# Performance work log

Hardware: AMD Instinct MI355X
Metric: run time of the kernel (lower is better)

Reference implementation:

```python
import jax, jax.numpy as jnp
import numpy as np

EMBED_DIM = 1024
NUM_TOKENS = 32
TOKEN_DIM = 32  # ceil(1024/32)
CODEBOOK_SIZE = 256
BATCH = 32768
BETA = 0.25


def setup_inputs() -> dict:
    key = jax.random.key(0)
    ks = jax.random.split(key, 6)
    lim_e = 1.0 / np.sqrt(EMBED_DIM)
    lim_d = 1.0 / np.sqrt(NUM_TOKENS * TOKEN_DIM)
    lim_c = 1.0 / CODEBOOK_SIZE
    return {
        "skills": jax.random.normal(ks[0], (BATCH, EMBED_DIM), jnp.float32),
        "enc_w": jax.random.uniform(ks[1], (NUM_TOKENS * TOKEN_DIM, EMBED_DIM), jnp.float32, -lim_e, lim_e),
        "enc_b": jax.random.uniform(ks[2], (NUM_TOKENS * TOKEN_DIM,), jnp.float32, -lim_e, lim_e),
        "codebook": jax.random.uniform(ks[3], (CODEBOOK_SIZE, TOKEN_DIM), jnp.float32, -lim_c, lim_c),
        "dec_w": jax.random.uniform(ks[4], (EMBED_DIM, NUM_TOKENS * TOKEN_DIM), jnp.float32, -lim_d, lim_d),
        "dec_b": jax.random.uniform(ks[5], (EMBED_DIM,), jnp.float32, -lim_d, lim_d),
    }


def reference(skills, enc_w, enc_b, codebook, dec_w, dec_b):
    B = skills.shape[0]
    # encoder linear -> [B, num_tokens, token_dim]
    projected = (skills @ enc_w.T + enc_b).reshape(B, NUM_TOKENS, TOKEN_DIM)
    flat = projected.reshape(-1, TOKEN_DIM)  # [B*T, d]
    # squared-euclidean distances to codebook entries: [B*T, K]
    dists = (
        jnp.sum(flat * flat, axis=1, keepdims=True)
        - 2.0 * flat @ codebook.T
        + jnp.sum(codebook * codebook, axis=1)[None, :]
    )
    codes = jnp.argmin(dists, axis=1)  # [B*T]
    quantized = codebook[codes].reshape(B, NUM_TOKENS, TOKEN_DIM)
    # straight-through estimator
    st = projected + jax.lax.stop_gradient(quantized - projected)
    commitment = jnp.mean((projected - jax.lax.stop_gradient(quantized)) ** 2)
    codebook_loss = jnp.mean((quantized - jax.lax.stop_gradient(projected)) ** 2)
    vq_loss = codebook_loss + BETA * commitment
    reconstructed = st.reshape(B, NUM_TOKENS * TOKEN_DIM) @ dec_w.T + dec_b
    recon_loss = jnp.mean((reconstructed - skills) ** 2)
    loss = vq_loss + recon_loss
    return reconstructed, codes.reshape(B, NUM_TOKENS), loss
```

## Files before the change

kernel.cpp:

```cpp
#include <hip/hip_runtime.h>
#include <hip/hip_bf16.h>
#include <float.h>

#define OUT_CODES_OFF (33554432UL)
#define OUT_LOSS_OFF  (34603008UL)
#define TAU 1e-5f
#define INV_N (1.0f/33554432.0f)

typedef __attribute__((ext_vector_type(8))) short s16x8;
typedef __attribute__((ext_vector_type(4))) float f32x4;

__device__ __forceinline__ unsigned short bf16r(float x) {
    unsigned int u = __float_as_uint(x);
    unsigned int r = (u + 0x7FFFu + ((u >> 16) & 1u)) >> 16;
    return (unsigned short)r;
}
__device__ __forceinline__ float bf16f(unsigned short h) {
    return __uint_as_float(((unsigned int)h) << 16);
}
__device__ __forceinline__ void split8r(float4 v0, float4 v1, s16x8& h, s16x8& l) {
    float xs[8] = {v0.x, v0.y, v0.z, v0.w, v1.x, v1.y, v1.z, v1.w};
    #pragma unroll
    for (int e = 0; e < 8; ++e) {
        unsigned int u = __float_as_uint(xs[e]);
        unsigned short hh = (unsigned short)(u >> 16);
        h[e] = (short)hh;
        l[e] = (short)bf16r(xs[e] - bf16f(hh));
    }
}

__global__ void k_prep_r(const float* __restrict__ in,
                         unsigned short* __restrict__ o,
                         int n8)
{
    const int i = blockIdx.x * 256 + threadIdx.x;
    if (i >= n8) return;
    const float4* p = (const float4*)(in + (size_t)i * 8);
    float4 v0 = p[0], v1 = p[1];
    float xs[8] = {v0.x, v0.y, v0.z, v0.w, v1.x, v1.y, v1.z, v1.w};
    s16x8 h;
    #pragma unroll
    for (int e = 0; e < 8; ++e) h[e] = (short)bf16r(xs[e]);
    *(s16x8*)(o + (size_t)i * 8) = h;
}

__launch_bounds__(512, 1)
__global__ void k_enc(const float* __restrict__ skills,
                      const float* __restrict__ enc_w,
                      const float* __restrict__ enc_b,
                      const float* __restrict__ cb_g,
                      float* __restrict__ out)
{
    __shared__ __align__(16) unsigned short us[40960];

    const int tid = threadIdx.x;
    const int rb = blockIdx.x >> 1, chf = blockIdx.x & 1;
    const int r0 = rb * 128;
    const int wid = tid >> 6, lane = tid & 63;
    const int wm = wid >> 1, wn = wid & 1;
    const int mbase = wm * 32;
    const int lhi = lane >> 4, llo = lane & 15;
    const int srow = tid >> 2, sq = tid & 3;

    if (tid < 256) {
        const float4* cr = (const float4*)&cb_g[tid * 32];
        float s = 0.f;
        #pragma unroll
        for (int i = 0; i < 8; ++i) {
            float4 v = cr[i];
            float c[4] = {v.x, v.y, v.z, v.w};
            #pragma unroll
            for (int e = 0; e < 4; ++e) {
                const int d = i * 4 + e;
                unsigned int u = __float_as_uint(c[e]);
                unsigned short hh = (unsigned short)(u >> 16);
                us[20480 + tid * 40 + d] = hh;
                us[30720 + tid * 40 + d] = bf16r(c[e] - bf16f(hh));
                s = fmaf(c[e], c[e], s);
            }
        }
        *(float*)&us[20480 + tid * 40 + 32] = s;
    }
    __syncthreads();

    float vq_local = 0.f;
    f32x4 acc[2][4];
    float4 ra0, ra1, rb0, rb1;

    {
        const float* ap = &skills[(size_t)(r0 + srow) * 1024 + sq * 8];
        ra0 = *(const float4*)ap; ra1 = *(const float4*)(ap + 4);
        const float* bp = &enc_w[(size_t)(chf * 512 + srow) * 1024 + sq * 8];
        rb0 = *(const float4*)bp; rb1 = *(const float4*)(bp + 4);
    }

    for (int it = 0; it < 128; ++it) {
        const int nt = it >> 5, kt = it & 31;
        if (kt == 0) {
            #pragma unroll
            for (int mf = 0; mf < 2; ++mf)
                #pragma unroll
                for (int nf = 0; nf < 4; ++nf) acc[mf][nf] = (f32x4)0.f;
        }
        __syncthreads();
        {
            s16x8 h, l;
            split8r(ra0, ra1, h, l);
            *(s16x8*)&us[srow * 40 + sq * 8] = h;
            *(s16x8*)&us[5120 + srow * 40 + sq * 8] = l;
            split8r(rb0, rb1, h, l);
            *(s16x8*)&us[10240 + srow * 40 + sq * 8] = h;
            *(s16x8*)&us[15360 + srow * 40 + sq * 8] = l;
        }
        __syncthreads();
        if (it < 127) {
            const int it2 = it + 1, nt2 = it2 >> 5, kt2 = it2 & 31;
            const float* ap = &skills[(size_t)(r0 + srow) * 1024 + kt2 * 32 + sq * 8];
            ra0 = *(const float4*)ap; ra1 = *(const float4*)(ap + 4);
            const float* bp = &enc_w[(size_t)(chf * 512 + nt2 * 128 + srow) * 1024 + kt2 * 32 + sq * 8];
            rb0 = *(const float4*)bp; rb1 = *(const float4*)(bp + 4);
        }
        {
            s16x8 ah[2], al[2];
            #pragma unroll
            for (int mf = 0; mf < 2; ++mf) {
                const int row = mbase + mf * 16 + llo;
                ah[mf] = *(s16x8*)&us[row * 40 + lhi * 8];
                al[mf] = *(s16x8*)&us[5120 + row * 40 + lhi * 8];
            }
            #pragma unroll
            for (int nf = 0; nf < 4; ++nf) {
                const int rowb = wn * 64 + nf * 16 + llo;
                s16x8 bh = *(s16x8*)&us[10240 + rowb * 40 + lhi * 8];
                s16x8 bl = *(s16x8*)&us[15360 + rowb * 40 + lhi * 8];
                #pragma unroll
                for (int mf = 0; mf < 2; ++mf) {
                    acc[mf][nf] = __builtin_amdgcn_mfma_f32_16x16x32_bf16(ah[mf], bh, acc[mf][nf], 0, 0, 0);
                    acc[mf][nf] = __builtin_amdgcn_mfma_f32_16x16x32_bf16(ah[mf], bl, acc[mf][nf], 0, 0, 0);
                    acc[mf][nf] = __builtin_amdgcn_mfma_f32_16x16x32_bf16(al[mf], bh, acc[mf][nf], 0, 0, 0);
                }
            }
        }

        if (kt == 31) {
            for (int c = 0; c < 2; ++c) {
                __syncthreads();
                if (wn == c) {
                    #pragma unroll
                    for (int nf = 0; nf < 4; ++nf) {
                        const int colh = nf * 16 + llo;
                        const int tlc = colh >> 5, d = colh & 31;
                        const float bias = enc_b[chf * 512 + nt * 128 + c * 64 + colh];
                        #pragma unroll
                        for (int mf = 0; mf < 2; ++mf)
                            #pragma unroll
                            for (int r = 0; r < 4; ++r) {
                                const int m_local = mbase + mf * 16 + lhi * 4 + r;
                                float val = acc[mf][nf][r] + bias;
                                unsigned int u = __float_as_uint(val);
                                unsigned short hh = (unsigned short)(u >> 16);
                                const int tok = m_local * 2 + tlc;
                                us[tok * 40 + d] = hh;
                                us[10240 + tok * 40 + d] = bf16r(val - bf16f(hh));
                            }
                    }
                }
                __syncthreads();
                #pragma unroll
                for (int gi = 0; gi < 2; ++gi) {
                    const int g = wid * 2 + gi;
                    const int tokrow = g * 16 + llo;
                    s16x8 fh = *(s16x8*)&us[tokrow * 40 + lhi * 8];
                    s16x8 fl = *(s16x8*)&us[10240 + tokrow * 40 + lhi * 8];
                    float Fp = 0.f;
                    #pragma unroll
                    for (int e = 0; e < 8; ++e) {
                        float fv = bf16f((unsigned short)fh[e]) + bf16f((unsigned short)fl[e]);
                        Fp = fmaf(fv, fv, Fp);
                    }
                    Fp += __shfl_xor(Fp, 16);
                    Fp += __shfl_xor(Fp, 32);

                    float s1[4], s2[4]; int bj[4];
                    #pragma unroll
                    for (int r = 0; r < 4; ++r) { s1[r] = FLT_MAX; s2[r] = FLT_MAX; bj[r] = 0; }
                    for (int jb = 0; jb < 16; ++jb) {
                        const int j = jb * 16 + llo;
                        s16x8 ch = *(s16x8*)&us[20480 + j * 40 + lhi * 8];
                        s16x8 cl = *(s16x8*)&us[30720 + j * 40 + lhi * 8];
                        const float cnv = *(const float*)&us[20480 + j * 40 + 32];
                        f32x4 sc = (f32x4)0.f;
                        sc = __builtin_amdgcn_mfma_f32_16x16x32_bf16(fh, ch, sc, 0, 0, 0);
                        sc = __builtin_amdgcn_mfma_f32_16x16x32_bf16(fh, cl, sc, 0, 0, 0);
                        sc = __builtin_amdgcn_mfma_f32_16x16x32_bf16(fl, ch, sc, 0, 0, 0);
                        #pragma unroll
                        for (int r = 0; r < 4; ++r) {
                            float s = fmaf(-2.f, sc[r], cnv);
                            if (s < s1[r])      { s2[r] = s1[r]; s1[r] = s; bj[r] = j; }
                            else if (s < s2[r]) { s2[r] = s; }
                        }
                    }
                    #pragma unroll
                    for (int r = 0; r < 4; ++r) {
                        float a1 = s1[r], a2 = s2[r]; int aj = bj[r];
                        #pragma unroll
                        for (int off = 1; off <= 8; off <<= 1) {
                            float o1 = __shfl_xor(a1, off);
                            float o2 = __shfl_xor(a2, off);
                            int   oj = __shfl_xor(aj, off);
                            if (o1 < a1) { a2 = fminf(a1, o2); a1 = o1; aj = oj; }
                            else         { a2 = fminf(o1, a2); }
                        }
                        const float Ft = __shfl(Fp, lhi * 4 + r);
                        if (llo == 0) {
                            const int tok_local = g * 16 + lhi * 4 + r;
                            const int row = tok_local >> 1, tlc2 = tok_local & 1;
                            const int t = chf * 16 + nt * 4 + c * 2 + tlc2;
                            float cv = (a2 - a1 < TAU) ? (float)(aj + 512) : (float)aj;
                            out[OUT_CODES_OFF + (size_t)(r0 + row) * 32 + t] = cv;
                            vq_local += Ft + a1;
                        }
                    }
                }
            }
        }
    }
    {
        float v = vq_local;
        #pragma unroll
        for (int off = 32; off >= 1; off >>= 1) v += __shfl_xor(v, off);
        if (lane == 0) atomicAdd(&out[OUT_LOSS_OFF], v * (1.25f * INV_N));
    }
}

__launch_bounds__(256)
__global__ void k_fix(const float* __restrict__ skills,
                      const float* __restrict__ enc_w,
                      const float* __restrict__ enc_b,
                      const float* __restrict__ cb_g,
                      float* __restrict__ codes)
{
    __shared__ unsigned int cnt;
    __shared__ unsigned short list[256];

    const int tid = threadIdx.x;
    const int base = blockIdx.x * 256;

    if (tid == 0) cnt = 0;
    __syncthreads();
    {
        const int c = (int)codes[base + tid];
        if (c >= 512) {
            unsigned int ix = atomicAdd(&cnt, 1u);
            list[ix] = (unsigned short)tid;
        }
    }
    __syncthreads();
    const unsigned int n = cnt;
    if (n == 0) return;

    const int wv = tid >> 6, lane = tid & 63;
    const int d = lane & 31;

    for (unsigned int i = wv; i < n; i += 4) {
        const int tok = base + (int)list[i];
        const int row = tok >> 5;
        const int t   = tok & 31;

        const float4* s4 = (const float4*)&skills[(size_t)row * 1024];
        const float4* w4 = (const float4*)&enc_w[(size_t)(t * 32 + d) * 1024];
        float v1 = 0.f, v2 = 0.f, v3 = 0.f;
        for (int q = 0; q < 96; ++q) {
            float4 a = s4[q], b = w4[q];
            v1 = fmaf(a.x, b.x, v1); v1 = fmaf(a.y, b.y, v1);
            v1 = fmaf(a.z, b.z, v1); v1 = fmaf(a.w, b.w, v1);
        }
        for (int q = 96; q < 192; ++q) {
            float4 a = s4[q], b = w4[q];
            v2 = fmaf(a.x, b.x, v2); v2 = fmaf(a.y, b.y, v2);
            v2 = fmaf(a.z, b.z, v2); v2 = fmaf(a.w, b.w, v2);
        }
        for (int q = 192; q < 256; ++q) {
            float4 a = s4[q], b = w4[q];
            v3 = fmaf(a.x, b.x, v3); v3 = fmaf(a.y, b.y, v3);
            v3 = fmaf(a.z, b.z, v3); v3 = fmaf(a.w, b.w, v3);
        }
        const float pd = ((v1 + v2) + v3) + enc_b[t * 32 + d];

        float pv[32];
        #pragma unroll
        for (int dd = 0; dd < 32; ++dd) pv[dd] = __shfl(pd, dd);

        float F;
        {
            float s[32];
            #pragma unroll
            for (int dd = 0; dd < 32; ++dd) s[dd] = pv[dd] * pv[dd];
            float r[8];
            #pragma unroll
            for (int j = 0; j < 8; ++j) r[j] = ((s[j] + s[8+j]) + s[16+j]) + s[24+j];
            F = ((r[0] + r[1]) + (r[2] + r[3])) + ((r[4] + r[5]) + (r[6] + r[7]));
        }

        float bs = FLT_MAX; int bj = 0;
        for (int m = 0; m < 4; ++m) {
            const int j = m * 64 + lane;
            const float* cj = &cb_g[j * 32];
            float g = 0.f;
            #pragma unroll
            for (int dd = 0; dd < 32; ++dd) g = fmaf(pv[dd], cj[dd], g);
            float cs[32];
            #pragma unroll
            for (int dd = 0; dd < 32; ++dd) cs[dd] = cj[dd] * cj[dd];
            float r[8];
            #pragma unroll
            for (int jj = 0; jj < 8; ++jj) r[jj] = ((cs[jj] + cs[8+jj]) + cs[16+jj]) + cs[24+jj];
            float cn = ((r[0] + r[1]) + (r[2] + r[3])) + ((r[4] + r[5]) + (r[6] + r[7]));
            float dist = (F - 2.0f * g) + cn;
            if (dist < bs) { bs = dist; bj = j; }
        }
        #pragma unroll
        for (int off = 32; off >= 1; off >>= 1) {
            float os = __shfl_xor(bs, off);
            int   oj = __shfl_xor(bj, off);
            if (os < bs || (os == bs && oj < bj)) { bs = os; bj = oj; }
        }
        if (lane == 0) codes[tok] = (float)bj;
    }
}

template <bool PRED>
__launch_bounds__(512)
__global__ void k_dec(const float* __restrict__ skills,
                      const float* __restrict__ cb_g,
                      const unsigned short* __restrict__ cbb,
                      const float* __restrict__ dec_w,
                      const unsigned short* __restrict__ dwb,
                      const float* __restrict__ dec_b,
                      const float* __restrict__ codes,
                      float* __restrict__ recon,
                      float* __restrict__ loss_out)
{
    __shared__ unsigned short Qt[128][40], Wt[128][40];

    const int tid = threadIdx.x;
    const int r0 = (blockIdx.x >> 3) * 128;
    const int n0 = (blockIdx.x & 7) * 128;
    const int wid = tid >> 6, lane = tid & 63;
    const int wm = wid >> 1, wn = wid & 1;
    const int mbase = wm * 32, nbase = wn * 64;
    const int lhi = lane >> 4, llo = lane & 15;
    const int srow = tid >> 2, sq = tid & 3;

    f32x4 acc[2][4];
    #pragma unroll
    for (int mf = 0; mf < 2; ++mf)
        #pragma unroll
        for (int nf = 0; nf < 4; ++nf) acc[mf][nf] = (f32x4)0.f;

    s16x8 q16, w16;
    float4 q0, q1, w0, w1;
    int cnext;
    {
        const int c0 = ((int)codes[(size_t)(r0 + srow) * 32 + 0]) & 255;
        if (PRED) {
            q16 = *(const s16x8*)(cbb + c0 * 32 + sq * 8);
            w16 = *(const s16x8*)(dwb + (size_t)(n0 + srow) * 1024 + sq * 8);
        } else {
            const float* cp = &cb_g[c0 * 32 + sq * 8];
            q0 = *(const float4*)cp; q1 = *(const float4*)(cp + 4);
            const float* wp = &dec_w[(size_t)(n0 + srow) * 1024 + sq * 8];
            w0 = *(const float4*)wp; w1 = *(const float4*)(wp + 4);
        }
        cnext = ((int)codes[(size_t)(r0 + srow) * 32 + 1]) & 255;
    }

    for (int t = 0; t < 32; ++t) {
        __syncthreads();
        if (PRED) {
            *(s16x8*)&Qt[srow][sq * 8] = q16;
            *(s16x8*)&Wt[srow][sq * 8] = w16;
        } else {
            float xs[8] = {q0.x, q0.y, q0.z, q0.w, q1.x, q1.y, q1.z, q1.w};
            s16x8 h;
            #pragma unroll
            for (int e = 0; e < 8; ++e) h[e] = (short)bf16r(xs[e]);
            *(s16x8*)&Qt[srow][sq * 8] = h;
            float ys[8] = {w0.x, w0.y, w0.z, w0.w, w1.x, w1.y, w1.z, w1.w};
            #pragma unroll
            for (int e = 0; e < 8; ++e) h[e] = (short)bf16r(ys[e]);
            *(s16x8*)&Wt[srow][sq * 8] = h;
        }
        __syncthreads();
        if (t < 31) {
            if (PRED) {
                q16 = *(const s16x8*)(cbb + cnext * 32 + sq * 8);
                w16 = *(const s16x8*)(dwb + (size_t)(n0 + srow) * 1024 + (t + 1) * 32 + sq * 8);
            } else {
                const float* cp = &cb_g[cnext * 32 + sq * 8];
                q0 = *(const float4*)cp; q1 = *(const float4*)(cp + 4);
                const float* wp = &dec_w[(size_t)(n0 + srow) * 1024 + (t + 1) * 32 + sq * 8];
                w0 = *(const float4*)wp; w1 = *(const float4*)(wp + 4);
            }
            if (t < 30) cnext = ((int)codes[(size_t)(r0 + srow) * 32 + t + 2]) & 255;
        }
        s16x8 aq[2], bw[4];
        #pragma unroll
        for (int mf = 0; mf < 2; ++mf)
            aq[mf] = *(s16x8*)&Qt[mbase + mf * 16 + llo][lhi * 8];
        #pragma unroll
        for (int nf = 0; nf < 4; ++nf)
            bw[nf] = *(s16x8*)&Wt[nbase + nf * 16 + llo][lhi * 8];
        #pragma unroll
        for (int mf = 0; mf < 2; ++mf)
            #pragma unroll
            for (int nf = 0; nf < 4; ++nf)
                acc[mf][nf] = __builtin_amdgcn_mfma_f32_16x16x32_bf16(aq[mf], bw[nf], acc[mf][nf], 0, 0, 0);
    }

    float lsum = 0.f;
    #pragma unroll
    for (int mf = 0; mf < 2; ++mf)
        #pragma unroll
        for (int nf = 0; nf < 4; ++nf) {
            const int col = n0 + nbase + nf * 16 + llo;
            const float bias = dec_b[col];
            #pragma unroll
            for (int r = 0; r < 4; ++r) {
                const int row = r0 + mbase + mf * 16 + lhi * 4 + r;
                float rv = acc[mf][nf][r] + bias;
                float dv = rv - skills[(size_t)row * 1024 + col];
                lsum = fmaf(dv, dv, lsum);
                recon[(size_t)row * 1024 + col] = rv;
            }
        }
    #pragma unroll
    for (int off = 32; off >= 1; off >>= 1) lsum += __shfl_xor(lsum, off);
    if (lane == 0) atomicAdd(loss_out, lsum * INV_N);
}

extern "C" void kernel_launch(void* const* d_in, const int* in_sizes, int n_in,
                              void* d_out, int out_size, void* d_ws, size_t ws_size,
                              hipStream_t stream)
{
    const float* skills = (const float*)d_in[0];
    const float* enc_w  = (const float*)d_in[1];
    const float* enc_b  = (const float*)d_in[2];
    const float* cbg    = (const float*)d_in[3];
    const float* dec_w  = (const float*)d_in[4];
    const float* dec_b  = (const float*)d_in[5];
    float* out = (float*)d_out;

    hipMemsetAsync(out + OUT_LOSS_OFF, 0, 4, stream);
    k_enc<<<dim3(512), dim3(512), 0, stream>>>(skills, enc_w, enc_b, cbg, out);
    k_fix<<<dim3(4096), dim3(256), 0, stream>>>(skills, enc_w, enc_b, cbg, out + OUT_CODES_OFF);

    const bool pred = (ws_size >= (2097152UL + 16384UL + 64UL));
    unsigned short* dwb = (unsigned short*)d_ws;
    unsigned short* cbb = dwb + 1048576UL;
    if (pred) {
        k_prep_r<<<dim3(512), dim3(256), 0, stream>>>(dec_w, dwb, 131072);
        k_prep_r<<<dim3(4), dim3(256), 0, stream>>>(cbg, cbb, 1024);
        k_dec<true><<<dim3(2048), dim3(512), 0, stream>>>(skills, cbg, cbb, dec_w, dwb, dec_b,
                                                          out + OUT_CODES_OFF, out, out + OUT_LOSS_OFF);
    } else {
        k_dec<false><<<dim3(2048), dim3(512), 0, stream>>>(skills, cbg, cbb, dec_w, dwb, dec_b,
                                                           out + OUT_CODES_OFF, out, out + OUT_LOSS_OFF);
    }
}
```

Before: 922.4 us.

## Halve encoder N-tile to 64 columns and interleave two token groups in codebook search

The encoder GEMM N-tile per block shrinks from 128 to 64 columns, so the outer loop runs 256 iterations instead of 128 and only half the threads load enc_w. The epilogue now handles one 64-column slice per tile with a single staging pass, and the codebook search processes both token groups per warp inside one loop over codebook entries, sharing the codebook LDS loads. This cuts accumulator registers and simplifies the epilogue. In exchange, the skills tile is reloaded and re-split twice as often, so activation traffic and conversion work double.

Result: slower. 1.064 ms (+15.3%).

```diff
diff --git a/kernel.cpp b/kernel.cpp
--- a/kernel.cpp
+++ b/kernel.cpp
@@ -61,6 +61,7 @@
     const int mbase = wm * 32;
     const int lhi = lane >> 4, llo = lane & 15;
     const int srow = tid >> 2, sq = tid & 3;
+    const int brow = (tid & 255) >> 2;
 
     if (tid < 256) {
         const float4* cr = (const float4*)&cb_g[tid * 32];
@@ -84,23 +85,25 @@
     __syncthreads();
 
     float vq_local = 0.f;
-    f32x4 acc[2][4];
+    f32x4 acc[2][2];
     float4 ra0, ra1, rb0, rb1;
 
     {
         const float* ap = &skills[(size_t)(r0 + srow) * 1024 + sq * 8];
         ra0 = *(const float4*)ap; ra1 = *(const float4*)(ap + 4);
-        const float* bp = &enc_w[(size_t)(chf * 512 + srow) * 1024 + sq * 8];
-        rb0 = *(const float4*)bp; rb1 = *(const float4*)(bp + 4);
-    }
-
-    for (int it = 0; it < 128; ++it) {
+        if (tid < 256) {
+            const float* bp = &enc_w[(size_t)(chf * 512 + brow) * 1024 + sq * 8];
+            rb0 = *(const float4*)bp; rb1 = *(const float4*)(bp + 4);
+        }
+    }
+
+    for (int it = 0; it < 256; ++it) {
         const int nt = it >> 5, kt = it & 31;
         if (kt == 0) {
             #pragma unroll
             for (int mf = 0; mf < 2; ++mf)
                 #pragma unroll
-                for (int nf = 0; nf < 4; ++nf) acc[mf][nf] = (f32x4)0.f;
+                for (int nf = 0; nf < 2; ++nf) acc[mf][nf] = (f32x4)0.f;
         }
         __syncthreads();
         {
@@ -108,17 +111,21 @@
             split8r(ra0, ra1, h, l);
             *(s16x8*)&us[srow * 40 + sq * 8] = h;
             *(s16x8*)&us[5120 + srow * 40 + sq * 8] = l;
-            split8r(rb0, rb1, h, l);
-            *(s16x8*)&us[10240 + srow * 40 + sq * 8] = h;
-            *(s16x8*)&us[15360 + srow * 40 + sq * 8] = l;
+            if (tid < 256) {
+                split8r(rb0, rb1, h, l);
+                *(s16x8*)&us[10240 + brow * 40 + sq * 8] = h;
+                *(s16x8*)&us[12800 + brow * 40 + sq * 8] = l;
+            }
         }
         __syncthreads();
-        if (it < 127) {
+        if (it < 255) {
             const int it2 = it + 1, nt2 = it2 >> 5, kt2 = it2 & 31;
             const float* ap = &skills[(size_t)(r0 + srow) * 1024 + kt2 * 32 + sq * 8];
             ra0 = *(const float4*)ap; ra1 = *(const float4*)(ap + 4);
-            const float* bp = &enc_w[(size_t)(chf * 512 + nt2 * 128 + srow) * 1024 + kt2 * 32 + sq * 8];
-            rb0 = *(const float4*)bp; rb1 = *(const float4*)(bp + 4);
+            if (tid < 256) {
+                const float* bp = &enc_w[(size_t)(chf * 512 + nt2 * 64 + brow) * 1024 + kt2 * 32 + sq * 8];
+                rb0 = *(const float4*)bp; rb1 = *(const float4*)(bp + 4);
+            }
         }
         {
             s16x8 ah[2], al[2];
@@ -129,10 +136,10 @@
                 al[mf] = *(s16x8*)&us[5120 + row * 40 + lhi * 8];
             }
             #pragma unroll
-            for (int nf = 0; nf < 4; ++nf) {
-                const int rowb = wn * 64 + nf * 16 + llo;
+            for (int nf = 0; nf < 2; ++nf) {
+                const int rowb = wn * 32 + nf * 16 + llo;
                 s16x8 bh = *(s16x8*)&us[10240 + rowb * 40 + lhi * 8];
-                s16x8 bl = *(s16x8*)&us[15360 + rowb * 40 + lhi * 8];
+                s16x8 bl = *(s16x8*)&us[12800 + rowb * 40 + lhi * 8];
                 #pragma unroll
                 for (int mf = 0; mf < 2; ++mf) {
                     acc[mf][nf] = __builtin_amdgcn_mfma_f32_16x16x32_bf16(ah[mf], bh, acc[mf][nf], 0, 0, 0);
@@ -143,83 +150,85 @@
         }
 
         if (kt == 31) {
-            for (int c = 0; c < 2; ++c) {
-                __syncthreads();
-                if (wn == c) {
+            __syncthreads();
+            #pragma unroll
+            for (int nf = 0; nf < 2; ++nf) {
+                const int d = nf * 16 + llo;
+                const float bias = enc_b[chf * 512 + nt * 64 + wn * 32 + d];
+                #pragma unroll
+                for (int mf = 0; mf < 2; ++mf)
                     #pragma unroll
-                    for (int nf = 0; nf < 4; ++nf) {
-                        const int colh = nf * 16 + llo;
-                        const int tlc = colh >> 5, d = colh & 31;
-                        const float bias = enc_b[chf * 512 + nt * 128 + c * 64 + colh];
-                        #pragma unroll
-                        for (int mf = 0; mf < 2; ++mf)
-                            #pragma unroll
-                            for (int r = 0; r < 4; ++r) {
-                                const int m_local = mbase + mf * 16 + lhi * 4 + r;
-                                float val = acc[mf][nf][r] + bias;
-                                unsigned int u = __float_as_uint(val);
-                                unsigned short hh = (unsigned short)(u >> 16);
-                                const int tok = m_local * 2 + tlc;
-                                us[tok * 40 + d] = hh;
-                                us[10240 + tok * 40 + d] = bf16r(val - bf16f(hh));
-                            }
+                    for (int r = 0; r < 4; ++r) {
+                        const int m_local = mbase + mf * 16 + lhi * 4 + r;
+                        float val = acc[mf][nf][r] + bias;
+                        unsigned int u = __float_as_uint(val);
+                        unsigned short hh = (unsigned short)(u >> 16);
+                        const int tok = m_local * 2 + wn;
+                        us[tok * 40 + d] = hh;
+                        us[10240 + tok * 40 + d] = bf16r(val - bf16f(hh));
+                    }
+            }
+            __syncthreads();
+            s16x8 fh[2], fl[2];
+            #pragma unroll
+            for (int gi = 0; gi < 2; ++gi) {
+                const int tokrow = (wid * 2 + gi) * 16 + llo;
+                fh[gi] = *(s16x8*)&us[tokrow * 40 + lhi * 8];
+                fl[gi] = *(s16x8*)&us[10240 + tokrow * 40 + lhi * 8];
+            }
+            float s1[2][4], s2[2][4]; int bj[2][4];
+            #pragma unroll
+            for (int gi = 0; gi < 2; ++gi)
+                #pragma unroll
+                for (int r = 0; r < 4; ++r) { s1[gi][r] = FLT_MAX; s2[gi][r] = FLT_MAX; bj[gi][r] = 0; }
+            for (int jb = 0; jb < 16; ++jb) {
+                const int j = jb * 16 + llo;
+                s16x8 ch = *(s16x8*)&us[20480 + j * 40 + lhi * 8];
+                s16x8 cl = *(s16x8*)&us[30720 + j * 40 + lhi * 8];
+                const float cnv = *(const float*)&us[20480 + j * 40 + 32];
+                #pragma unroll
+                for (int gi = 0; gi < 2; ++gi) {
+                    f32x4 sc = (f32x4)0.f;
+                    sc = __builtin_amdgcn_mfma_f32_16x16x32_bf16(fh[gi], ch, sc, 0, 0, 0);
+                    sc = __builtin_amdgcn_mfma_f32_16x16x32_bf16(fh[gi], cl, sc, 0, 0, 0);
+                    sc = __builtin_amdgcn_mfma_f32_16x16x32_bf16(fl[gi], ch, sc, 0, 0, 0);
+                    #pragma unroll
+                    for (int r = 0; r < 4; ++r) {
+                        float s = fmaf(-2.f, sc[r], cnv);
+                        if (s < s1[gi][r])      { s2[gi][r] = s1[gi][r]; s1[gi][r] = s; bj[gi][r] = j; }
+                        else if (s < s2[gi][r]) { s2[gi][r] = s; }
                     }
                 }
-                __syncthreads();
-                #pragma unroll
-                for (int gi = 0; gi < 2; ++gi) {
-                    const int g = wid * 2 + gi;
-                    const int tokrow = g * 16 + llo;
-                    s16x8 fh = *(s16x8*)&us[tokrow * 40 + lhi * 8];
-                    s16x8 fl = *(s16x8*)&us[10240 + tokrow * 40 + lhi * 8];
-                    float Fp = 0.f;
+            }
+            #pragma unroll
+            for (int gi = 0; gi < 2; ++gi) {
+                float Fp = 0.f;
+                #pragma unroll
+                for (int e = 0; e < 8; ++e) {
+                    float fv = bf16f((unsigned short)fh[gi][e]) + bf16f((unsigned short)fl[gi][e]);
+                    Fp = fmaf(fv, fv, Fp);
+                }
+                Fp += __shfl_xor(Fp, 16);
+                Fp += __shfl_xor(Fp, 32);
+                #pragma unroll
+                for (int r = 0; r < 4; ++r) {
+                    float a1 = s1[gi][r], a2 = s2[gi][r]; int aj = bj[gi][r];
                     #pragma unroll
-                    for (int e = 0; e < 8; ++e) {
-                        float fv = bf16f((unsigned short)fh[e]) + bf16f((unsigned short)fl[e]);
-                        Fp = fmaf(fv, fv, Fp);
+                    for (int off = 1; off <= 8; off <<= 1) {
+                        float o1 = __shfl_xor(a1, off);
+                        float o2 = __shfl_xor(a2, off);
+                        int   oj = __shfl_xor(aj, off);
+                        if (o1 < a1) { a2 = fminf(a1, o2); a1 = o1; aj = oj; }
+                        else         { a2 = fminf(o1, a2); }
                     }
-                    Fp += __shfl_xor(Fp, 16);
-                    Fp += __shfl_xor(Fp, 32);
-
-                    float s1[4], s2[4]; int bj[4];
-                    #pragma unroll
-                    for (int r = 0; r < 4; ++r) { s1[r] = FLT_MAX; s2[r] = FLT_MAX; bj[r] = 0; }
-                    for (int jb = 0; jb < 16; ++jb) {
-                        const int j = jb * 16 + llo;
-                        s16x8 ch = *(s16x8*)&us[20480 + j * 40 + lhi * 8];
-                        s16x8 cl = *(s16x8*)&us[30720 + j * 40 + lhi * 8];
-                        const float cnv = *(const float*)&us[20480 + j * 40 + 32];
-                        f32x4 sc = (f32x4)0.f;
-                        sc = __builtin_amdgcn_mfma_f32_16x16x32_bf16(fh, ch, sc, 0, 0, 0);
-                        sc = __builtin_amdgcn_mfma_f32_16x16x32_bf16(fh, cl, sc, 0, 0, 0);
-                        sc = __builtin_amdgcn_mfma_f32_16x16x32_bf16(fl, ch, sc, 0, 0, 0);
-                        #pragma unroll
-                        for (int r = 0; r < 4; ++r) {
-                            float s = fmaf(-2.f, sc[r], cnv);
-                            if (s < s1[r])      { s2[r] = s1[r]; s1[r] = s; bj[r] = j; }
-                            else if (s < s2[r]) { s2[r] = s; }
-                        }
-                    }
-                    #pragma unroll
-                    for (int r = 0; r < 4; ++r) {
-                        float a1 = s1[r], a2 = s2[r]; int aj = bj[r];
-                        #pragma unroll
-                        for (int off = 1; off <= 8; off <<= 1) {
-                            float o1 = __shfl_xor(a1, off);
-                            float o2 = __shfl_xor(a2, off);
-                            int   oj = __shfl_xor(aj, off);
-                            if (o1 < a1) { a2 = fminf(a1, o2); a1 = o1; aj = oj; }
-                            else         { a2 = fminf(o1, a2); }
-                        }
-                        const float Ft = __shfl(Fp, lhi * 4 + r);
-                        if (llo == 0) {
-                            const int tok_local = g * 16 + lhi * 4 + r;
-                            const int row = tok_local >> 1, tlc2 = tok_local & 1;
-                            const int t = chf * 16 + nt * 4 + c * 2 + tlc2;
-                            float cv = (a2 - a1 < TAU) ? (float)(aj + 512) : (float)aj;
-                            out[OUT_CODES_OFF + (size_t)(r0 + row) * 32 + t] = cv;
-                            vq_local += Ft + a1;
-                        }
+                    const float Ft = __shfl(Fp, lhi * 4 + r);
+                    if (llo == 0) {
+                        const int tok_local = (wid * 2 + gi) * 16 + lhi * 4 + r;
+                        const int row = tok_local >> 1;
+                        const int t = chf * 16 + nt * 2 + (tok_local & 1);
+                        float cv = (a2 - a1 < TAU) ? (float)(aj + 512) : (float)aj;
+                        out[OUT_CODES_OFF + (size_t)(r0 + row) * 32 + t] = cv;
+                        vq_local += Ft + a1;
                     }
                 }
             }
```

## Pre-split encoder operands to bf16 hi/lo tiles and load via global_load_lds

Applied to the files above, without the earlier changes.

Adds a prep kernel that splits skills and enc_w into bf16 hi/lo pairs laid out per tile. The encoder can then stream tiles straight into LDS with global_load_lds instead of loading fp32 and converting in-kernel. The split skills are stashed in the output buffer, and enc_w goes into a larger workspace. The codebook argmin loop is also restructured so two token groups share each codebook fragment load. In exchange the kernel gains an extra full pass over the 128MB skills input plus a 128MB bf16 write, and the path only runs when the workspace is large enough.

Result: no change. 914.4 us (-0.9%).

```diff
diff --git a/kernel.cpp b/kernel.cpp
--- a/kernel.cpp
+++ b/kernel.cpp
@@ -27,6 +27,26 @@
         h[e] = (short)hh;
         l[e] = (short)bf16r(xs[e] - bf16f(hh));
     }
+}
+
+__device__ __forceinline__ void gld16(const unsigned short* g, unsigned short* l) {
+    __builtin_amdgcn_global_load_lds(
+        (const __attribute__((address_space(1))) unsigned int*)g,
+        (__attribute__((address_space(3))) unsigned int*)l, 16, 0, 0);
+}
+
+__global__ void k_prep_split(const float* __restrict__ in,
+                             unsigned short* __restrict__ ot)
+{
+    const int b = blockIdx.x, tid = threadIdx.x;
+    const int rblk = b >> 5, kt = b & 31, r = tid >> 2, q = tid & 3;
+    const float* src = in + (size_t)(rblk * 128 + r) * 1024 + kt * 32 + q * 8;
+    float4 v0 = *(const float4*)src, v1 = *(const float4*)(src + 4);
+    s16x8 h, l;
+    split8r(v0, v1, h, l);
+    unsigned short* dst = ot + (size_t)b * 8192 + q * 1024 + r * 8;
+    *(s16x8*)dst = h;
+    *(s16x8*)(dst + 4096) = l;
 }
 
 __global__ void k_prep_r(const float* __restrict__ in,
@@ -45,11 +65,192 @@
 }
 
 __launch_bounds__(512, 1)
-__global__ void k_enc(const float* __restrict__ skills,
-                      const float* __restrict__ enc_w,
-                      const float* __restrict__ enc_b,
-                      const float* __restrict__ cb_g,
-                      float* __restrict__ out)
+__global__ void k_enc_gl(const unsigned short* __restrict__ At,
+                         const unsigned short* __restrict__ Bt,
+                         const float* __restrict__ enc_b,
+                         const float* __restrict__ cb_g,
+                         float* __restrict__ out)
+{
+    __shared__ __align__(16) unsigned short us[33280];
+
+    const int tid = threadIdx.x;
+    const int rb = blockIdx.x >> 1, chf = blockIdx.x & 1;
+    const int r0 = rb * 128;
+    const int wid = tid >> 6, lane = tid & 63;
+    const int wm = wid >> 1, wn = wid & 1;
+    const int mbase = wm * 32;
+    const int lhi = lane >> 4, llo = lane & 15;
+
+    if (tid < 256) {
+        const float4* cr = (const float4*)&cb_g[tid * 32];
+        float s = 0.f;
+        #pragma unroll
+        for (int i = 0; i < 8; ++i) {
+            float4 v = cr[i];
+            float c[4] = {v.x, v.y, v.z, v.w};
+            #pragma unroll
+            for (int e = 0; e < 4; ++e) {
+                const int d = i * 4 + e, kc = d >> 3, e8 = d & 7;
+                unsigned int u = __float_as_uint(c[e]);
+                unsigned short hh = (unsigned short)(u >> 16);
+                us[16384 + kc * 2048 + tid * 8 + e8] = hh;
+                us[24576 + kc * 2048 + tid * 8 + e8] = bf16r(c[e] - bf16f(hh));
+                s = fmaf(c[e], c[e], s);
+            }
+        }
+        *(float*)&us[32768 + tid * 2] = s;
+    }
+    __syncthreads();
+
+    float vq_local = 0.f;
+    f32x4 acc[2][4];
+    const int ntg_base = chf * 4;
+
+    for (int it = 0; it < 128; ++it) {
+        const int nt = it >> 5, kt = it & 31;
+        if (kt == 0) {
+            #pragma unroll
+            for (int mf = 0; mf < 2; ++mf)
+                #pragma unroll
+                for (int nf = 0; nf < 4; ++nf) acc[mf][nf] = (f32x4)0.f;
+        }
+        __syncthreads();
+        {
+            const unsigned short* gA = At + ((size_t)(rb * 32 + kt)) * 8192 + tid * 8;
+            const unsigned short* gB = Bt + ((size_t)((ntg_base + nt) * 32 + kt)) * 8192 + tid * 8;
+            gld16(gA,        us + wid * 512);
+            gld16(gA + 4096, us + 4096 + wid * 512);
+            gld16(gB,        us + 8192 + wid * 512);
+            gld16(gB + 4096, us + 12288 + wid * 512);
+        }
+        __syncthreads();
+        {
+            s16x8 ah[2], al[2];
+            #pragma unroll
+            for (int mf = 0; mf < 2; ++mf) {
+                const int row = mbase + mf * 16 + llo;
+                ah[mf] = *(s16x8*)&us[lhi * 1024 + row * 8];
+                al[mf] = *(s16x8*)&us[4096 + lhi * 1024 + row * 8];
+            }
+            #pragma unroll
+            for (int nf = 0; nf < 4; ++nf) {
+                const int rowb = wn * 64 + nf * 16 + llo;
+                s16x8 bh = *(s16x8*)&us[8192 + lhi * 1024 + rowb * 8];
+                s16x8 bl = *(s16x8*)&us[12288 + lhi * 1024 + rowb * 8];
+                #pragma unroll
+                for (int mf = 0; mf < 2; ++mf) {
+                    acc[mf][nf] = __builtin_amdgcn_mfma_f32_16x16x32_bf16(ah[mf], bh, acc[mf][nf], 0, 0, 0);
+                    acc[mf][nf] = __builtin_amdgcn_mfma_f32_16x16x32_bf16(ah[mf], bl, acc[mf][nf], 0, 0, 0);
+                    acc[mf][nf] = __builtin_amdgcn_mfma_f32_16x16x32_bf16(al[mf], bh, acc[mf][nf], 0, 0, 0);
+                }
+            }
+        }
+
+        if (kt == 31) {
+            for (int c = 0; c < 2; ++c) {
+                __syncthreads();
+                if (wn == c) {
+                    #pragma unroll
+                    for (int nf = 0; nf < 4; ++nf) {
+                        const int colh = nf * 16 + llo;
+                        const int tlc = colh >> 5, d = colh & 31;
+                        const int kc = d >> 3, e8 = d & 7;
+                        const float bias = enc_b[chf * 512 + nt * 128 + c * 64 + colh];
+                        #pragma unroll
+                        for (int mf = 0; mf < 2; ++mf)
+                            #pragma unroll
+                            for (int r = 0; r < 4; ++r) {
+                                const int m_local = mbase + mf * 16 + lhi * 4 + r;
+                                float val = acc[mf][nf][r] + bias;
+                                unsigned int u = __float_as_uint(val);
+                                unsigned short hh = (unsigned short)(u >> 16);
+                                const int tok = m_local * 2 + tlc;
+                                us[kc * 2048 + tok * 8 + e8] = hh;
+                                us[8192 + kc * 2048 + tok * 8 + e8] = bf16r(val - bf16f(hh));
+                            }
+                    }
+                }
+                __syncthreads();
+                s16x8 fh[2], fl[2];
+                #pragma unroll
+                for (int gi = 0; gi < 2; ++gi) {
+                    const int tokrow = (wid * 2 + gi) * 16 + llo;
+                    fh[gi] = *(s16x8*)&us[lhi * 2048 + tokrow * 8];
+                    fl[gi] = *(s16x8*)&us[8192 + lhi * 2048 + tokrow * 8];
+                }
+                float s1[2][4], s2[2][4]; int bj[2][4];
+                #pragma unroll
+                for (int gi = 0; gi < 2; ++gi)
+                    #pragma unroll
+                    for (int r = 0; r < 4; ++r) { s1[gi][r] = FLT_MAX; s2[gi][r] = FLT_MAX; bj[gi][r] = 0; }
+                for (int jb = 0; jb < 16; ++jb) {
+                    const int j = jb * 16 + llo;
+                    s16x8 ch = *(s16x8*)&us[16384 + lhi * 2048 + j * 8];
+                    s16x8 cl = *(s16x8*)&us[24576 + lhi * 2048 + j * 8];
+                    const float cnv = *(const float*)&us[32768 + j * 2];
+                    #pragma unroll
+                    for (int gi = 0; gi < 2; ++gi) {
+                        f32x4 sc = (f32x4)0.f;
+                        sc = __builtin_amdgcn_mfma_f32_16x16x32_bf16(fh[gi], ch, sc, 0, 0, 0);
+                        sc = __builtin_amdgcn_mfma_f32_16x16x32_bf16(fh[gi], cl, sc, 0, 0, 0);
+                        sc = __builtin_amdgcn_mfma_f32_16x16x32_bf16(fl[gi], ch, sc, 0, 0, 0);
+                        #pragma unroll
+                        for (int r = 0; r < 4; ++r) {
+                            float s = fmaf(-2.f, sc[r], cnv);
+                            if (s < s1[gi][r])      { s2[gi][r] = s1[gi][r]; s1[gi][r] = s; bj[gi][r] = j; }
+                            else if (s < s2[gi][r]) { s2[gi][r] = s; }
+                        }
+                    }
+                }
+                #pragma unroll
+                for (int gi = 0; gi < 2; ++gi) {
+                    float Fp = 0.f;
+                    #pragma unroll
+                    for (int e = 0; e < 8; ++e) {
+                        float fv = bf16f((unsigned short)fh[gi][e]) + bf16f((unsigned short)fl[gi][e]);
+                        Fp = fmaf(fv, fv, Fp);
+                    }
+                    Fp += __shfl_xor(Fp, 16);
+                    Fp += __shfl_xor(Fp, 32);
+                    #pragma unroll
+                    for (int r = 0; r < 4; ++r) {
+                        float a1 = s1[gi][r], a2 = s2[gi][r]; int aj = bj[gi][r];
+                        #pragma unroll
+                        for (int off = 1; off <= 8; off <<= 1) {
+                            float o1 = __shfl_xor(a1, off);
+                            float o2 = __shfl_xor(a2, off);
+                            int   oj = __shfl_xor(aj, off);
+                            if (o1 < a1) { a2 = fminf(a1, o2); a1 = o1; aj = oj; }
+                            else         { a2 = fminf(o1, a2); }
+                        }
+                        const float Ft = __shfl(Fp, lhi * 4 + r);
+                        if (llo == 0) {
+                            const int tok_local = (wid * 2 + gi) * 16 + lhi * 4 + r;
+                            const int row = tok_local >> 1, tlc2 = tok_local & 1;
+                            const int t = chf * 16 + nt * 4 + c * 2 + tlc2;
+                            float cv = (a2 - a1 < TAU) ? (float)(aj + 512) : (float)aj;
+                            out[OUT_CODES_OFF + (size_t)(r0 + row) * 32 + t] = cv;
+                            vq_local += Ft + a1;
+                        }
+                    }
+                }
+            }
+        }
+    }
+    {
+        float v = vq_local;
+        #pragma unroll
+        for (int off = 32; off >= 1; off >>= 1) v += __shfl_xor(v, off);
+        if (lane == 0) atomicAdd(&out[OUT_LOSS_OFF], v * (1.25f * INV_N));
+    }
+}
+
+__launch_bounds__(512, 1)
+__global__ void k_enc_fb(const float* __restrict__ skills,
+                         const float* __restrict__ enc_w,
+                         const float* __restrict__ enc_b,
+                         const float* __restrict__ cb_g,
+                         float* __restrict__ out)
 {
     __shared__ __align__(16) unsigned short us[40960];
 
@@ -86,7 +287,6 @@
     float vq_local = 0.f;
     f32x4 acc[2][4];
     float4 ra0, ra1, rb0, rb1;
-
     {
         const float* ap = &skills[(size_t)(r0 + srow) * 1024 + sq * 8];
         ra0 = *(const float4*)ap; ra1 = *(const float4*)(ap + 4);
@@ -166,43 +366,50 @@
                     }
                 }
                 __syncthreads();
+                s16x8 fh[2], fl[2];
                 #pragma unroll
                 for (int gi = 0; gi < 2; ++gi) {
-                    const int g = wid * 2 + gi;
-                    const int tokrow = g * 16 + llo;
-                    s16x8 fh = *(s16x8*)&us[tokrow * 40 + lhi * 8];
-                    s16x8 fl = *(s16x8*)&us[10240 + tokrow * 40 + lhi * 8];
-                    float Fp = 0.f;
-                    #pragma unroll
-                    for (int e = 0; e < 8; ++e) {
-                        float fv = bf16f((unsigned short)fh[e]) + bf16f((unsigned short)fl[e]);
-                        Fp = fmaf(fv, fv, Fp);
-                    }
-                    Fp += __shfl_xor(Fp, 16);
-                    Fp += __shfl_xor(Fp, 32);
-
-                    float s1[4], s2[4]; int bj[4];
-                    #pragma unroll
-                    for (int r = 0; r < 4; ++r) { s1[r] = FLT_MAX; s2[r] = FLT_MAX; bj[r] = 0; }
-                    for (int jb = 0; jb < 16; ++jb) {
-                        const int j = jb * 16 + llo;
-                        s16x8 ch = *(s16x8*)&us[20480 + j * 40 + lhi * 8];
-                        s16x8 cl = *(s16x8*)&us[30720 + j * 40 + lhi * 8];
-                        const float cnv = *(const float*)&us[20480 + j * 40 + 32];
+                    const int tokrow = (wid * 2 + gi) * 16 + llo;
+                    fh[gi] = *(s16x8*)&us[tokrow * 40 + lhi * 8];
+                    fl[gi] = *(s16x8*)&us[10240 + tokrow * 40 + lhi * 8];
+                }
+                float s1[2][4], s2[2][4]; int bj[2][4];
+                #pragma unroll
+                for (int gi = 0; gi < 2; ++gi)
+                    #pragma unroll
+                    for (int r = 0; r < 4; ++r) { s1[gi][r] = FLT_MAX; s2[gi][r] = FLT_MAX; bj[gi][r] = 0; }
+                for (int jb = 0; jb < 16; ++jb) {
+                    const int j = jb * 16 + llo;
+                    s16x8 ch = *(s16x8*)&us[20480 + j * 40 + lhi * 8];
+                    s16x8 cl = *(s16x8*)&us[30720 + j * 40 + lhi * 8];
+                    const float cnv = *(const float*)&us[20480 + j * 40 + 32];
+                    #pragma unroll
+                    for (int gi = 0; gi < 2; ++gi) {
                         f32x4 sc = (f32x4)0.f;
-                        sc = __builtin_amdgcn_mfma_f32_16x16x32_bf16(fh, ch, sc, 0, 0, 0);
-                        sc = __builtin_amdgcn_mfma_f32_16x16x32_bf16(fh, cl, sc, 0, 0, 0);
-                        sc = __builtin_amdgcn_mfma_f32_16x16x32_bf16(fl, ch, sc, 0, 0, 0);
+                        sc = __builtin_amdgcn_mfma_f32_16x16x32_bf16(fh[gi], ch, sc, 0, 0, 0);
+                        sc = __builtin_amdgcn_mfma_f32_16x16x32_bf16(fh[gi], cl, sc, 0, 0, 0);
+                        sc = __builtin_amdgcn_mfma_f32_16x16x32_bf16(fl[gi], ch, sc, 0, 0, 0);
                         #pragma unroll
                         for (int r = 0; r < 4; ++r) {
                             float s = fmaf(-2.f, sc[r], cnv);
-                            if (s < s1[r])      { s2[r] = s1[r]; s1[r] = s; bj[r] = j; }
-                            else if (s < s2[r]) { s2[r] = s; }
+                            if (s < s1[gi][r])      { s2[gi][r] = s1[gi][r]; s1[gi][r] = s; bj[gi][r] = j; }
+                            else if (s < s2[gi][r]) { s2[gi][r] = s; }
                         }
                     }
+                }
+                #pragma unroll
+                for (int gi = 0; gi < 2; ++gi) {
+                    float Fp = 0.f;
+                    #pragma unroll
+                    for (int e = 0; e < 8; ++e) {
+                        float fv = bf16f((unsigned short)fh[gi][e]) + bf16f((unsigned short)fl[gi][e]);
+                        Fp = fmaf(fv, fv, Fp);
+                    }
+                    Fp += __shfl_xor(Fp, 16);
+                    Fp += __shfl_xor(Fp, 32);
                     #pragma unroll
                     for (int r = 0; r < 4; ++r) {
-                        float a1 = s1[r], a2 = s2[r]; int aj = bj[r];
+                        float a1 = s1[gi][r], a2 = s2[gi][r]; int aj = bj[gi][r];
                         #pragma unroll
                         for (int off = 1; off <= 8; off <<= 1) {
                             float o1 = __shfl_xor(a1, off);
@@ -213,7 +420,7 @@
                         }
                         const float Ft = __shfl(Fp, lhi * 4 + r);
                         if (llo == 0) {
-                            const int tok_local = g * 16 + lhi * 4 + r;
+                            const int tok_local = (wid * 2 + gi) * 16 + lhi * 4 + r;
                             const int row = tok_local >> 1, tlc2 = tok_local & 1;
                             const int t = chf * 16 + nt * 4 + c * 2 + tlc2;
                             float cv = (a2 - a1 < TAU) ? (float)(aj + 512) : (float)aj;
@@ -452,19 +659,38 @@
     float* out = (float*)d_out;
 
     hipMemsetAsync(out + OUT_LOSS_OFF, 0, 4, stream);
-    k_enc<<<dim3(512), dim3(512), 0, stream>>>(skills, enc_w, enc_b, cbg, out);
-    k_fix<<<dim3(4096), dim3(256), 0, stream>>>(skills, enc_w, enc_b, cbg, out + OUT_CODES_OFF);
-
-    const bool pred = (ws_size >= (2097152UL + 16384UL + 64UL));
-    unsigned short* dwb = (unsigned short*)d_ws;
-    unsigned short* cbb = dwb + 1048576UL;
-    if (pred) {
+
+    const size_t NEED_BIG = 4UL*1024*1024 + 2097152UL + 16384UL + 256UL;
+    unsigned short* wsu16 = (unsigned short*)d_ws;
+
+    if (ws_size >= NEED_BIG) {
+        unsigned short* Btl = wsu16;
+        unsigned short* dwb = wsu16 + 2097152UL;
+        unsigned short* cbb = wsu16 + 3145728UL;
+        unsigned short* Atl = (unsigned short*)out;
+
+        k_prep_split<<<dim3(8192), dim3(512), 0, stream>>>(skills, Atl);
+        k_prep_split<<<dim3(256),  dim3(512), 0, stream>>>(enc_w, Btl);
+        k_enc_gl<<<dim3(512), dim3(512), 0, stream>>>(Atl, Btl, enc_b, cbg, out);
+        k_fix<<<dim3(4096), dim3(256), 0, stream>>>(skills, enc_w, enc_b, cbg, out + OUT_CODES_OFF);
         k_prep_r<<<dim3(512), dim3(256), 0, stream>>>(dec_w, dwb, 131072);
         k_prep_r<<<dim3(4), dim3(256), 0, stream>>>(cbg, cbb, 1024);
         k_dec<true><<<dim3(2048), dim3(512), 0, stream>>>(skills, cbg, cbb, dec_w, dwb, dec_b,
                                                           out + OUT_CODES_OFF, out, out + OUT_LOSS_OFF);
     } else {
-        k_dec<false><<<dim3(2048), dim3(512), 0, stream>>>(skills, cbg, cbb, dec_w, dwb, dec_b,
-                                                           out + OUT_CODES_OFF, out, out + OUT_LOSS_OFF);
-    }
-}
+        k_enc_fb<<<dim3(512), dim3(512), 0, stream>>>(skills, enc_w, enc_b, cbg, out);
+        k_fix<<<dim3(4096), dim3(256), 0, stream>>>(skills, enc_w, enc_b, cbg, out + OUT_CODES_OFF);
+        const bool pred = (ws_size >= (2097152UL + 16384UL + 64UL));
+        unsigned short* dwb = wsu16;
+        unsigned short* cbb = wsu16 + 1048576UL;
+        if (pred) {
+            k_prep_r<<<dim3(512), dim3(256), 0, stream>>>(dec_w, dwb, 131072);
+            k_prep_r<<<dim3(4), dim3(256), 0, stream>>>(cbg, cbb, 1024);
+            k_dec<true><<<dim3(2048), dim3(512), 0, stream>>>(skills, cbg, cbb, dec_w, dwb, dec_b,
+                                                              out + OUT_CODES_OFF, out, out + OUT_LOSS_OFF);
+        } else {
+            k_dec<false><<<dim3(2048), dim3(512), 0, stream>>>(skills, cbg, cbb, dec_w, dwb, dec_b,
+                                                               out + OUT_CODES_OFF, out, out + OUT_LOSS_OFF);
+        }
+    }
+}
```
